# Optimization experiments

Measured on AMD Instinct MI355X. Metric: run time of the kernel, lower is better.

Reference implementation:

```python
import jax, jax.numpy as jnp
import numpy as np

# Protocol constants (config.protocol); standard DCE-MRI values.
TR = 0.005                       # repetition time [s]
ALPHA = 15.0 / 180.0 * np.pi     # flip angle [rad]
DELTT = 4.0 / 60.0               # temporal resolution [min]
R1_RELAX = 4.5                   # contrast agent relaxivity [/mM/s]
N_TIME = 112
BATCH = 262144


def setup_inputs() -> dict:
    key = jax.random.key(0)
    k1, k2, k3, k4, k5 = jax.random.split(key, 5)
    # Physiologically plausible positive ranges (avoid division blowups).
    ktrans = jax.random.uniform(k1, (BATCH, 1), jnp.float32, 0.01, 1.0)
    vp = jax.random.uniform(k2, (BATCH, 1), jnp.float32, 0.0, 0.1)
    ve = jax.random.uniform(k3, (BATCH, 1), jnp.float32, 0.05, 1.0)
    T10 = jax.random.uniform(k4, (BATCH, 1), jnp.float32, 0.5, 2.0)
    CAp = jax.random.uniform(k5, (BATCH, N_TIME), jnp.float32, 0.0, 1.0)
    return {"ktrans": ktrans, "vp": vp, "ve": ve, "T10": T10, "CAp": CAp}


def _cae(CAp, ktrans, ve):
    # Original: Toeplitz matrix ce_x with ce[b,i] = ktrans*deltt *
    #   sum_{j<=i} CAp[b,j] * exp(-ktrans/ve * (i-j) * deltt)
    # == first-order IIR recurrence c_i = decay * c_{i-1} + CAp[:, i].
    decay = jnp.exp(-ktrans / ve * DELTT)[:, 0]  # [B]

    def step(c, cap_t):
        c = c * decay + cap_t
        return c, c

    c0 = jnp.zeros(CAp.shape[0], CAp.dtype)
    _, cs = jax.lax.scan(step, c0, CAp.T)  # cs: [N, B]
    return (ktrans * DELTT) * cs.T          # [B, N]


def reference(ktrans, vp, ve, T10, CAp):
    ce = _cae(CAp, ktrans, ve)                 # [B, N]
    ct = vp * CAp + ce                         # tissue concentration
    R1t = 1.0 / T10 + R1_RELAX * ct            # [B, N]
    e = jnp.exp(-TR * R1t)
    s = (1.0 - e) * np.sin(ALPHA) / (1.0 - e * np.cos(ALPHA))
    return s * 20.0


if __name__ == "__main__":
    out = reference(**setup_inputs())
    print(out.shape, out.dtype)
```

## Files before the change

### kernel.cpp

```cpp
#include <hip/hip_runtime.h>

#define N_TIME  112
#define BATCH   262144
#define NF4ROW  28
#define NCH     7
#define RPW     16
#define LP      29

__device__ __forceinline__ float sig(float cap, float c, float vp,
                                     float kd, float invT10) {
    const float TR     = 0.005f;
    const float R1     = 4.5f;
    const float SINA20 = 20.0f * 0.25881904510252074f;
    const float COSA   = 0.96592582628906829f;
    float ct = vp * cap + kd * c;
    float e  = __expf(-TR * (invT10 + R1 * ct));
    return (1.0f - e) * SINA20 * __builtin_amdgcn_rcpf(1.0f - e * COSA);
}

__global__ __launch_bounds__(256) void etofts_kernel(
    const float* __restrict__ ktrans_p,
    const float* __restrict__ vp_p,
    const float* __restrict__ ve_p,
    const float* __restrict__ T10_p,
    const float* __restrict__ cap_p,
    float* __restrict__ out_p)
{
    __shared__ float4 tile[4][RPW * LP];

    const int w    = threadIdx.x >> 6;
    const int lane = threadIdx.x & 63;
    const int g0   = blockIdx.x * 64 + w * RPW;

    float4* wt = tile[w];

    const float4* src = reinterpret_cast<const float4*>(cap_p) + (size_t)g0 * NF4ROW;
    float4*       dst = reinterpret_cast<float4*>(out_p)       + (size_t)g0 * NF4ROW;

    float4 ld[NCH];
    int    slot[NCH];
    #pragma unroll
    for (int k = 0; k < NCH; ++k) {
        int f   = lane + (k << 6);
        ld[k]   = src[f];
        slot[k] = (f / NF4ROW) * LP + (f % NF4ROW);
    }

    const int r    = lane >> 2;
    const int t    = lane & 3;
    const int grow = g0 + r;

    const float DELTT  = 4.0f / 60.0f;
    const float ktrans = ktrans_p[grow];
    const float vp     = vp_p[grow];
    const float ve     = ve_p[grow];
    const float invT10 = __builtin_amdgcn_rcpf(T10_p[grow]);
    const float kd     = ktrans * DELTT;

    const float d1  = __expf(-ktrans / ve * DELTT);
    const float d2  = d1 * d1;
    const float d3  = d2 * d1;
    const float d4  = d2 * d2;
    const float d8  = d4 * d4;
    const float d12 = d8 * d4;
    const float d16 = d8 * d8;
    const float dt4 = (t == 0) ? 1.0f : (t == 1) ? d4 : (t == 2) ? d8 : d12;

    #pragma unroll
    for (int k = 0; k < NCH; ++k) wt[slot[k]] = ld[k];

    float4 x[NCH];
    #pragma unroll
    for (int ch = 0; ch < NCH; ++ch) x[ch] = wt[r * LP + ch * 4 + t];

    float s1[NCH], s2[NCH], s3[NCH], E[NCH], T[NCH];
    #pragma unroll
    for (int ch = 0; ch < NCH; ++ch) {
        float a0 = x[ch].x;
        float a1 = fmaf(d1, a0, x[ch].y);
        float a2 = fmaf(d1, a1, x[ch].z);
        float a3 = fmaf(d1, a2, x[ch].w);
        s1[ch] = a1; s2[ch] = a2; s3[ch] = a3;

        float S  = a3;
        float v1 = __shfl_up(S, 1, 4);
        if (t >= 1) S = fmaf(d4, v1, S);
        float v2 = __shfl_up(S, 2, 4);
        if (t >= 2) S = fmaf(d8, v2, S);

        E[ch] = __shfl_up(S, 1, 4);
        T[ch] = __shfl(S, 3, 4);
    }

    float C[NCH];
    C[0] = 0.0f;
    #pragma unroll
    for (int ch = 0; ch < NCH - 1; ++ch) C[ch + 1] = fmaf(d16, C[ch], T[ch]);

    #pragma unroll
    for (int ch = 0; ch < NCH; ++ch) {
        float tin = (t == 0) ? dt4 * C[ch] : fmaf(dt4, C[ch], E[ch]);

        float c0 = fmaf(d1, tin, x[ch].x);
        float c1 = fmaf(d2, tin, s1[ch]);
        float c2 = fmaf(d3, tin, s2[ch]);
        float c3 = fmaf(d4, tin, s3[ch]);

        float4 y;
        y.x = sig(x[ch].x, c0, vp, kd, invT10);
        y.y = sig(x[ch].y, c1, vp, kd, invT10);
        y.z = sig(x[ch].z, c2, vp, kd, invT10);
        y.w = sig(x[ch].w, c3, vp, kd, invT10);
        wt[r * LP + ch * 4 + t] = y;
    }

    #pragma unroll
    for (int k = 0; k < NCH; ++k) dst[lane + (k << 6)] = wt[slot[k]];
}

extern "C" void kernel_launch(void* const* d_in, const int* in_sizes, int n_in,
                              void* d_out, int out_size, void* d_ws, size_t ws_size,
                              hipStream_t stream) {
    const float* ktrans = (const float*)d_in[0];
    const float* vp     = (const float*)d_in[1];
    const float* ve     = (const float*)d_in[2];
    const float* T10    = (const float*)d_in[3];
    const float* CAp    = (const float*)d_in[4];
    float* out = (float*)d_out;

    dim3 block(256);
    dim3 grid(BATCH / 64);
    etofts_kernel<<<grid, block, 0, stream>>>(ktrans, vp, ve, T10, CAp, out);
}
```

Measured before the change: 40.80 us.

## Process four row groups per wave with software-prefetched loads

Each wave now handles four consecutive 16-row groups in an unrolled loop instead of one, and issues the global loads for the next group before computing the current one. The grid shrinks by a factor of four, and launch bounds request four blocks per SM. The aim is to hide memory latency in a bandwidth-bound kernel and amortise launch and block overhead. In exchange, register pressure rises and the number of waves available to hide latency drops.

```diff
diff --git a/kernel.cpp b/kernel.cpp
--- a/kernel.cpp
+++ b/kernel.cpp
@@ -5,6 +5,7 @@
 #define NF4ROW  28
 #define NCH     7
 #define RPW     16
+#define W       4
 #define LP      29
 
 __device__ __forceinline__ float sig(float cap, float c, float vp,
@@ -18,7 +19,7 @@
     return (1.0f - e) * SINA20 * __builtin_amdgcn_rcpf(1.0f - e * COSA);
 }
 
-__global__ __launch_bounds__(256) void etofts_kernel(
+__global__ __launch_bounds__(256, 4) void etofts_kernel(
     const float* __restrict__ ktrans_p,
     const float* __restrict__ vp_p,
     const float* __restrict__ ve_p,
@@ -30,92 +31,118 @@
 
     const int w    = threadIdx.x >> 6;
     const int lane = threadIdx.x & 63;
-    const int g0   = blockIdx.x * 64 + w * RPW;
+    const int r    = lane >> 2;
+    const int t    = lane & 3;
+    const int wb   = blockIdx.x * 256 + w * 64;
 
     float4* wt = tile[w];
 
-    const float4* src = reinterpret_cast<const float4*>(cap_p) + (size_t)g0 * NF4ROW;
-    float4*       dst = reinterpret_cast<float4*>(out_p)       + (size_t)g0 * NF4ROW;
-
-    float4 ld[NCH];
-    int    slot[NCH];
+    int slot[NCH];
     #pragma unroll
     for (int k = 0; k < NCH; ++k) {
         int f   = lane + (k << 6);
-        ld[k]   = src[f];
         slot[k] = (f / NF4ROW) * LP + (f % NF4ROW);
     }
 
-    const int r    = lane >> 2;
-    const int t    = lane & 3;
-    const int grow = g0 + r;
+    const float4* capv = reinterpret_cast<const float4*>(cap_p);
+    float4*       outv = reinterpret_cast<float4*>(out_p);
 
-    const float DELTT  = 4.0f / 60.0f;
-    const float ktrans = ktrans_p[grow];
-    const float vp     = vp_p[grow];
-    const float ve     = ve_p[grow];
-    const float invT10 = __builtin_amdgcn_rcpf(T10_p[grow]);
-    const float kd     = ktrans * DELTT;
+    const float DELTT = 4.0f / 60.0f;
 
-    const float d1  = __expf(-ktrans / ve * DELTT);
-    const float d2  = d1 * d1;
-    const float d3  = d2 * d1;
-    const float d4  = d2 * d2;
-    const float d8  = d4 * d4;
-    const float d12 = d8 * d4;
-    const float d16 = d8 * d8;
-    const float dt4 = (t == 0) ? 1.0f : (t == 1) ? d4 : (t == 2) ? d8 : d12;
+    float4 ld[NCH];
+    {
+        const float4* s0 = capv + (size_t)wb * NF4ROW;
+        #pragma unroll
+        for (int k = 0; k < NCH; ++k) ld[k] = s0[lane + (k << 6)];
+    }
+    float pk = ktrans_p[wb + r];
+    float pv = vp_p[wb + r];
+    float pe = ve_p[wb + r];
+    float pT = T10_p[wb + r];
+    float npk, npv, npe, npT;
 
     #pragma unroll
-    for (int k = 0; k < NCH; ++k) wt[slot[k]] = ld[k];
+    for (int s = 0; s < W; ++s) {
+        const int row0 = wb + s * RPW;
 
-    float4 x[NCH];
-    #pragma unroll
-    for (int ch = 0; ch < NCH; ++ch) x[ch] = wt[r * LP + ch * 4 + t];
+        #pragma unroll
+        for (int k = 0; k < NCH; ++k) wt[slot[k]] = ld[k];
 
-    float s1[NCH], s2[NCH], s3[NCH], E[NCH], T[NCH];
-    #pragma unroll
-    for (int ch = 0; ch < NCH; ++ch) {
-        float a0 = x[ch].x;
-        float a1 = fmaf(d1, a0, x[ch].y);
-        float a2 = fmaf(d1, a1, x[ch].z);
-        float a3 = fmaf(d1, a2, x[ch].w);
-        s1[ch] = a1; s2[ch] = a2; s3[ch] = a3;
+        if (s + 1 < W) {
+            const float4* sn = capv + (size_t)(row0 + RPW) * NF4ROW;
+            #pragma unroll
+            for (int k = 0; k < NCH; ++k) ld[k] = sn[lane + (k << 6)];
+            npk = ktrans_p[row0 + RPW + r];
+            npv = vp_p[row0 + RPW + r];
+            npe = ve_p[row0 + RPW + r];
+            npT = T10_p[row0 + RPW + r];
+        }
 
-        float S  = a3;
-        float v1 = __shfl_up(S, 1, 4);
-        if (t >= 1) S = fmaf(d4, v1, S);
-        float v2 = __shfl_up(S, 2, 4);
-        if (t >= 2) S = fmaf(d8, v2, S);
+        const float ktrans = pk, vp = pv, ve = pe;
+        const float invT10 = __builtin_amdgcn_rcpf(pT);
+        const float kd     = ktrans * DELTT;
+        const float d1  = __expf(-ktrans / ve * DELTT);
+        const float d2  = d1 * d1;
+        const float d3  = d2 * d1;
+        const float d4  = d2 * d2;
+        const float d8  = d4 * d4;
+        const float d12 = d8 * d4;
+        const float d16 = d8 * d8;
+        const float dt4 = (t == 0) ? 1.0f : (t == 1) ? d4 : (t == 2) ? d8 : d12;
 
-        E[ch] = __shfl_up(S, 1, 4);
-        T[ch] = __shfl(S, 3, 4);
+        float4 x[NCH];
+        #pragma unroll
+        for (int ch = 0; ch < NCH; ++ch) x[ch] = wt[r * LP + ch * 4 + t];
+
+        float s1[NCH], s2[NCH], s3[NCH], E[NCH], T[NCH];
+        #pragma unroll
+        for (int ch = 0; ch < NCH; ++ch) {
+            float a0 = x[ch].x;
+            float a1 = fmaf(d1, a0, x[ch].y);
+            float a2 = fmaf(d1, a1, x[ch].z);
+            float a3 = fmaf(d1, a2, x[ch].w);
+            s1[ch] = a1; s2[ch] = a2; s3[ch] = a3;
+
+            float S  = a3;
+            float v1 = __shfl_up(S, 1, 4);
+            if (t >= 1) S = fmaf(d4, v1, S);
+            float v2 = __shfl_up(S, 2, 4);
+            if (t >= 2) S = fmaf(d8, v2, S);
+
+            E[ch] = __shfl_up(S, 1, 4);
+            T[ch] = __shfl(S, 3, 4);
+        }
+
+        float C[NCH];
+        C[0] = 0.0f;
+        #pragma unroll
+        for (int ch = 0; ch < NCH - 1; ++ch) C[ch + 1] = fmaf(d16, C[ch], T[ch]);
+
+        #pragma unroll
+        for (int ch = 0; ch < NCH; ++ch) {
+            float tin = (t == 0) ? dt4 * C[ch] : fmaf(dt4, C[ch], E[ch]);
+
+            float c0 = fmaf(d1, tin, x[ch].x);
+            float c1 = fmaf(d2, tin, s1[ch]);
+            float c2 = fmaf(d3, tin, s2[ch]);
+            float c3 = fmaf(d4, tin, s3[ch]);
+
+            float4 y;
+            y.x = sig(x[ch].x, c0, vp, kd, invT10);
+            y.y = sig(x[ch].y, c1, vp, kd, invT10);
+            y.z = sig(x[ch].z, c2, vp, kd, invT10);
+            y.w = sig(x[ch].w, c3, vp, kd, invT10);
+            wt[r * LP + ch * 4 + t] = y;
+        }
+
+        {
+            float4* dn = outv + (size_t)row0 * NF4ROW;
+            #pragma unroll
+            for (int k = 0; k < NCH; ++k) dn[lane + (k << 6)] = wt[slot[k]];
+        }
+
+        if (s + 1 < W) { pk = npk; pv = npv; pe = npe; pT = npT; }
     }
-
-    float C[NCH];
-    C[0] = 0.0f;
-    #pragma unroll
-    for (int ch = 0; ch < NCH - 1; ++ch) C[ch + 1] = fmaf(d16, C[ch], T[ch]);
-
-    #pragma unroll
-    for (int ch = 0; ch < NCH; ++ch) {
-        float tin = (t == 0) ? dt4 * C[ch] : fmaf(dt4, C[ch], E[ch]);
-
-        float c0 = fmaf(d1, tin, x[ch].x);
-        float c1 = fmaf(d2, tin, s1[ch]);
-        float c2 = fmaf(d3, tin, s2[ch]);
-        float c3 = fmaf(d4, tin, s3[ch]);
-
-        float4 y;
-        y.x = sig(x[ch].x, c0, vp, kd, invT10);
-        y.y = sig(x[ch].y, c1, vp, kd, invT10);
-        y.z = sig(x[ch].z, c2, vp, kd, invT10);
-        y.w = sig(x[ch].w, c3, vp, kd, invT10);
-        wt[r * LP + ch * 4 + t] = y;
-    }
-
-    #pragma unroll
-    for (int k = 0; k < NCH; ++k) dst[lane + (k << 6)] = wt[slot[k]];
 }
 
 extern "C" void kernel_launch(void* const* d_in, const int* in_sizes, int n_in,
@@ -129,6 +156,6 @@
     float* out = (float*)d_out;
 
     dim3 block(256);
-    dim3 grid(BATCH / 64);
+    dim3 grid(BATCH / 256);
     etofts_kernel<<<grid, block, 0, stream>>>(ktrans, vp, ve, T10, CAp, out);
 }
```

After: 41.66 us. 2.1% more time.
